# Kernel optimization log

Hardware: AMD Instinct MI355X
Metric: run time of the kernel (lower is better)

## Reference

```python
import jax, jax.numpy as jnp
import numpy as np

BINS = 6  # torch.histc(bins=6, min=0, max=256) in rarity()


def _border_mask(h, w, dtype):
    m = jnp.ones((h, w), dtype)
    return m.at[0, :].set(0).at[-1, :].set(0).at[:, 0].set(0).at[:, -1].set(0)


def _norm(x, lo, hi, axes):
    # normalize_tensor: map to [lo,hi]; all-zeros if constant map
    mn = x.min(axes, keepdims=True)
    mx = x.max(axes, keepdims=True)
    d = mx - mn
    ds = jnp.where(d == 0, jnp.ones_like(d), d)
    out = (x - mn) / ds * (hi - lo) + lo
    return jnp.where(d == 0, jnp.zeros_like(out), out)


def _ponder(x, axes):
    # map_ponderation: normalize to [0,1] then scale by (max-mean)^2
    w = (x.max(axes, keepdims=True) - x.mean(axes, keepdims=True)) ** 2
    return _norm(x, 0.0, 1.0, axes) * w


def _rarity_all(ch):
    # Vectorized rarity() over all channels. ch: [C,H,W]
    C, H, W = ch.shape
    ch = ch * _border_mask(H, W, ch.dtype)          # zero 1-px border
    ch = _norm(ch, 0.0, 256.0, (1, 2))              # per-channel -> [0,256]
    # torch.histc over [0,256]: bin = floor(v*bins/256), max value in last bin
    bin_idx = jnp.clip((ch * (BINS / 256.0)).astype(jnp.int32), 0, BINS - 1)
    hist = jax.nn.one_hot(bin_idx, BINS, dtype=ch.dtype).sum((1, 2))  # [C,BINS]
    hist = hist / hist.sum(-1, keepdims=True)
    hist = -jnp.log(hist + 1e-4)
    # lookup: (channel*bins - 1).long().clamp(0, bins-1)  (channel in [0,256], as in source)
    lut_idx = jnp.clip((ch * BINS - 1).astype(jnp.int32), 0, BINS - 1)
    dst = hist[jnp.arange(C)[:, None, None], lut_idx]  # [C,H,W] rarity lookup
    dst = _norm(dst, 0.0, 1.0, (1, 2))
    return _ponder(dst, (1, 2))


def _apply_rarity(x):
    # x: [1,C,H,W] -> [H,W]
    ch = x[0]
    H, W = ch.shape[-2:]
    r = _rarity_all(ch)
    # channel 0: ponderated again, no extra border zeroing (as in source)
    p0 = _ponder(r[0], (0, 1))
    rest = r[1:] * _border_mask(H, W, r.dtype)  # channels 1..C-1: border zeroed
    p = p0 + _ponder(rest, (1, 2)).sum(0)
    return _norm(p, 0.0, 1.0, (0, 1))  # threshold=None -> no thresholding


def _resize240(m):
    # T.Resize((240,240), bilinear) ~ half-pixel linear resize
    return jax.image.resize(m, (240, 240), method='linear')


def _forward(layers):
    # group layers into packs by spatial resolution (static, shapes known)
    packs = {}
    for t in layers:
        packs.setdefault(t.shape[-2:], []).append(t)
    group_maps = []
    for pack in packs.values():
        maps = [_resize240(_apply_rarity(t)) for t in pack]
        fused = maps[0] * 0.0
        for m in maps:  # fuse_itti
            fused = fused + _ponder(m, (0, 1))
        group_maps.append(_norm(fused, 0.0, 256.0, (0, 1)))
    groups = jnp.stack(group_maps, -1)  # [240,240,n_packs]
    return groups.sum(-1), groups


def setup_inputs() -> dict:
    key = jax.random.key(0)
    shapes = ([(1, 64, 224, 224)] * 2 + [(1, 128, 112, 112)] * 2 +
              [(1, 256, 56, 56)] * 3 + [(1, 512, 28, 28)] * 3 +
              [(1, 512, 14, 14)] * 3)
    keys = jax.random.split(key, len(shapes))
    return {f"x{i}": jax.random.uniform(keys[i], s, jnp.float32)
            for i, s in enumerate(shapes)}


def reference(x0, x1, x2, x3, x4, x5, x6, x7, x8, x9, x10, x11, x12):
    return _forward([x0, x1, x2, x3, x4, x5, x6, x7, x8, x9, x10, x11, x12])
```

## Files before the change

kernel.cpp:

```cpp
#include <hip/hip_runtime.h>
#include <math.h>

#define NT 13
#define RHW 57600
#define PIXB 8192

struct Meta {
  const float* x[NT];
  int C[NT];
  int H[NT];
  float hsc[NT];
  int pixOff[NT + 1];
  int mmOff[NT + 1];
  int nchMM[NT];
  int pmOff[NT + 1];
};

__device__ __forceinline__ int segOf(const int* off, int b) {
  int t = 0;
  while (t + 1 < NT && b >= off[t + 1]) t++;
  return t;
}

template <int HH>
__device__ __forceinline__ void mm_body(const float* __restrict__ ch, int pix0, int pix1, float& mn, float& mx) {
  constexpr int W = HH, H = HH;
  int i40 = pix0 >> 2, i41 = pix1 >> 2;
  for (int i4 = i40 + (int)threadIdx.x; i4 < i41; i4 += 256) {
    float4 v = reinterpret_cast<const float4*>(ch)[i4];
#pragma unroll
    for (int j = 0; j < 4; j++) {
      int idx = i4 * 4 + j;
      int h = idx / W, w = idx - h * W;
      bool ok = h > 0 && h < (H - 1) && w > 0 && w < (W - 1);
      float f = (j == 0) ? v.x : (j == 1) ? v.y : (j == 2) ? v.z : v.w;
      if (ok) { mn = fminf(mn, f); mx = fmaxf(mx, f); }
    }
  }
}

__global__ __launch_bounds__(256) void k_minmax(Meta m, float* cpart) {
  int b = blockIdx.x;
  int t = segOf(m.mmOff, b);
  int local = b - m.mmOff[t];
  int nch = m.nchMM[t];
  int c = local / nch, k = local - c * nch;
  int HW = m.H[t] * m.H[t];
  const float* ch = m.x[t] + (size_t)c * HW;
  int pix0 = k * PIXB, pix1 = min(pix0 + PIXB, HW);
  float mn = INFINITY, mx = -INFINITY;
  switch (m.H[t]) {
    case 224: mm_body<224>(ch, pix0, pix1, mn, mx); break;
    case 112: mm_body<112>(ch, pix0, pix1, mn, mx); break;
    case 56:  mm_body<56>(ch, pix0, pix1, mn, mx); break;
    case 28:  mm_body<28>(ch, pix0, pix1, mn, mx); break;
    default:  mm_body<14>(ch, pix0, pix1, mn, mx); break;
  }
#pragma unroll
  for (int o = 32; o > 0; o >>= 1) {
    mn = fminf(mn, __shfl_down(mn, o));
    mx = fmaxf(mx, __shfl_down(mx, o));
  }
  __shared__ float smn[4], smx[4];
  int wid = threadIdx.x >> 6;
  if ((threadIdx.x & 63) == 0) { smn[wid] = mn; smx[wid] = mx; }
  __syncthreads();
  if (threadIdx.x == 0) {
    for (int i = 1; i < 4; i++) { mn = fminf(mn, smn[i]); mx = fmaxf(mx, smx[i]); }
    cpart[2 * b] = mn; cpart[2 * b + 1] = mx;
  }
}

template <int HH>
__device__ __forceinline__ void hist_body(const float* __restrict__ ch, int pix0, int pix1,
                                          float mn, float invd,
                                          unsigned long long& cbin, unsigned long long& clut) {
  constexpr int W = HH, H = HH;
  int i40 = pix0 >> 2, i41 = pix1 >> 2;
  int nIter = (i41 - i40 + 255) >> 8;
  for (int it = 0; it < nIter; ++it) {
    int i4 = i40 + it * 256 + (int)threadIdx.x;
    bool valid = i4 < i41;
    float4 v = make_float4(0.f, 0.f, 0.f, 0.f);
    if (valid) v = reinterpret_cast<const float4*>(ch)[i4];
#pragma unroll
    for (int j = 0; j < 4; j++) {
      int idx = i4 * 4 + j;
      int h = idx / W, w = idx - h * W;
      bool ok = valid && h > 0 && h < (H - 1) && w > 0 && w < (W - 1);
      float f = (j == 0) ? v.x : (j == 1) ? v.y : (j == 2) ? v.z : v.w;
      float vv = (f - mn) * invd * 256.0f;
      int bin = (int)(vv * 0.0234375f);
      bin = bin < 0 ? 0 : (bin > 5 ? 5 : bin);
      float tt = vv * 6.0f - 1.0f;
      int li = (int)tt;
      li = li < 0 ? 0 : (li > 5 ? 5 : li);
      cbin += (unsigned long long)ok << (bin * 10);
      clut += (unsigned long long)ok << (li * 10);
    }
  }
}

__global__ __launch_bounds__(256) void k_hist(Meta m, const float* cpart, unsigned* hpart) {
  int b = blockIdx.x;
  int t = segOf(m.mmOff, b);
  int local = b - m.mmOff[t];
  int nch = m.nchMM[t];
  int c = local / nch, k = local - c * nch;
  int HW = m.H[t] * m.H[t];
  const float* ch = m.x[t] + (size_t)c * HW;
  int cb = m.mmOff[t] + c * nch;
  float mn = INFINITY, mx = -INFINITY;
  for (int kk = 0; kk < nch; kk++) {
    mn = fminf(mn, cpart[2 * (cb + kk)]);
    mx = fmaxf(mx, cpart[2 * (cb + kk) + 1]);
  }
  mn = fminf(mn, 0.f);
  mx = fmaxf(mx, 0.f);
  float d = mx - mn;
  float invd = d > 0.f ? 1.0f / d : 0.f;
  int pix0 = k * PIXB, pix1 = min(pix0 + PIXB, HW);
  unsigned long long cbin = 0ull, clut = 0ull;
  switch (m.H[t]) {
    case 224: hist_body<224>(ch, pix0, pix1, mn, invd, cbin, clut); break;
    case 112: hist_body<112>(ch, pix0, pix1, mn, invd, cbin, clut); break;
    case 56:  hist_body<56>(ch, pix0, pix1, mn, invd, cbin, clut); break;
    case 28:  hist_body<28>(ch, pix0, pix1, mn, invd, cbin, clut); break;
    default:  hist_body<14>(ch, pix0, pix1, mn, invd, cbin, clut); break;
  }
  unsigned pk[6];
#pragma unroll
  for (int j = 0; j < 6; j++)
    pk[j] = (unsigned)((cbin >> (10 * j)) & 1023ull) | ((unsigned)((clut >> (10 * j)) & 1023ull) << 16);
#pragma unroll
  for (int o = 32; o > 0; o >>= 1) {
#pragma unroll
    for (int j = 0; j < 6; j++) pk[j] += __shfl_down(pk[j], o);
  }
  __shared__ unsigned swh[4][12];
  int wid = threadIdx.x >> 6, lane = threadIdx.x & 63;
  if (lane == 0) {
#pragma unroll
    for (int j = 0; j < 6; j++) { swh[wid][j] = pk[j] & 0xffffu; swh[wid][6 + j] = pk[j] >> 16; }
  }
  __syncthreads();
  if (threadIdx.x < 12)
    hpart[12 * b + threadIdx.x] =
        swh[0][threadIdx.x] + swh[1][threadIdx.x] + swh[2][threadIdx.x] + swh[3][threadIdx.x];
}

template <int HH>
__device__ __forceinline__ void pm_inner(const float* __restrict__ X, int i4, bool act,
                                         int c0, int c1, const float* sLut,
                                         const float* sMn, const float* sInv, float* a) {
  constexpr int W = HH, H = HH;
  constexpr int i4n = (H * W) / 4;
  if (!act) return;
  int bf[4];
#pragma unroll
  for (int j = 0; j < 4; j++) {
    int idx = i4 * 4 + j;
    int h = idx / W, w = idx - h * W;
    bf[j] = (h == 0 || h == H - 1 || w == 0 || w == W - 1) ? 1 : 0;
  }
  const float4* Xp = reinterpret_cast<const float4*>(X);
#pragma unroll 4
  for (int c = c0; c < c1; ++c) {
    float4 v = Xp[(size_t)c * i4n + i4];
    float mnc = sMn[c], ivc = sInv[c];
    const float* L = sLut + c * 8;
    float fv0 = v.x, fv1 = v.y, fv2 = v.z, fv3 = v.w;
    { float vv = (fv0 - mnc) * ivc * 256.0f; float tt = vv * 6.0f - 1.0f; int li = (int)tt; li = li < 0 ? 0 : (li > 5 ? 5 : li); a[0] += L[bf[0] ? 6 : li]; }
    { float vv = (fv1 - mnc) * ivc * 256.0f; float tt = vv * 6.0f - 1.0f; int li = (int)tt; li = li < 0 ? 0 : (li > 5 ? 5 : li); a[1] += L[bf[1] ? 6 : li]; }
    { float vv = (fv2 - mnc) * ivc * 256.0f; float tt = vv * 6.0f - 1.0f; int li = (int)tt; li = li < 0 ? 0 : (li > 5 ? 5 : li); a[2] += L[bf[2] ? 6 : li]; }
    { float vv = (fv3 - mnc) * ivc * 256.0f; float tt = vv * 6.0f - 1.0f; int li = (int)tt; li = li < 0 ? 0 : (li > 5 ? 5 : li); a[3] += L[bf[3] ? 6 : li]; }
  }
}

__global__ __launch_bounds__(512) void k_pmap(Meta m, const float* cpart, const unsigned* hpart,
                                              float* pmaps, float* ppart) {
  __shared__ float sLut[512 * 8];
  __shared__ float sMn[512], sInv[512];
  __shared__ float sAcc[8][256];
  int b = blockIdx.x;
  int t = segOf(m.pmOff, b);
  int blk = b - m.pmOff[t];
  int C = m.C[t], H = m.H[t], W = H, HW = H * W;
  int nch = m.nchMM[t];
  int tid = threadIdx.x;
  if (tid < C) {
    int cb = m.mmOff[t] + tid * nch;
    float mn = INFINITY, mx = -INFINITY;
    unsigned hh[12];
#pragma unroll
    for (int j = 0; j < 12; j++) hh[j] = 0u;
    for (int k = 0; k < nch; k++) {
      mn = fminf(mn, cpart[2 * (cb + k)]);
      mx = fmaxf(mx, cpart[2 * (cb + k) + 1]);
#pragma unroll
      for (int j = 0; j < 12; j++) hh[j] += hpart[12 * (cb + k) + j];
    }
    mn = fminf(mn, 0.f); mx = fmaxf(mx, 0.f);
    float d = mx - mn;
    float invd = d > 0.f ? 1.0f / d : 0.f;
    float fHW = (float)HW;
    int nb = 2 * (H + W) - 4;
    float vb = (0.f - mn) * invd * 256.0f;
    int bin_b = (int)(vb * 0.0234375f);
    bin_b = bin_b < 0 ? 0 : (bin_b > 5 ? 5 : bin_b);
    float ttb = vb * 6.0f - 1.0f;
    int lib = (int)ttb;
    lib = lib < 0 ? 0 : (lib > 5 ? 5 : lib);
    hh[bin_b] += (unsigned)nb;
    hh[6 + lib] += (unsigned)nb;
    float hl[6];
#pragma unroll
    for (int j = 0; j < 6; j++) hl[j] = -logf((float)hh[j] / fHW + 1e-4f);
    float mn2 = INFINITY, mx2 = -INFINITY, sum2 = 0.f;
#pragma unroll
    for (int j = 0; j < 6; j++) {
      unsigned cc = hh[6 + j];
      if (cc) { mn2 = fminf(mn2, hl[j]); mx2 = fmaxf(mx2, hl[j]); sum2 += (float)cc * hl[j]; }
    }
    float d2 = mx2 - mn2;
    float RL[6];
    if (d2 > 0.f) {
      float meanN = (sum2 / fHW - mn2) / d2;
      float w = 1.0f - meanN; w *= w;
#pragma unroll
      for (int j = 0; j < 6; j++) RL[j] = (hl[j] - mn2) / d2 * w;
    } else {
#pragma unroll
      for (int j = 0; j < 6; j++) RL[j] = 0.f;
    }
    float LUT[7];
    if (tid == 0) {
      float mnr = INFINITY, mxr = -INFINITY, sumr = 0.f;
#pragma unroll
      for (int j = 0; j < 6; j++) {
        unsigned cc = hh[6 + j];
        if (cc) { mnr = fminf(mnr, RL[j]); mxr = fmaxf(mxr, RL[j]); sumr += (float)cc * RL[j]; }
      }
      float dr = mxr - mnr;
      if (dr > 0.f) {
        float meanr = sumr / fHW;
        float wp = mxr - meanr; wp *= wp;
#pragma unroll
        for (int j = 0; j < 6; j++) LUT[j] = (RL[j] - mnr) / dr * wp;
        LUT[6] = LUT[lib];
      } else {
#pragma unroll
        for (int j = 0; j < 7; j++) LUT[j] = 0.f;
      }
    } else {
      float mnr = 0.f, mxr = 0.f, sumr = 0.f;
#pragma unroll
      for (int j = 0; j < 6; j++) {
        int cc = (int)hh[6 + j] - (j == lib ? nb : 0);
        if (cc > 0) { mnr = fminf(mnr, RL[j]); mxr = fmaxf(mxr, RL[j]); sumr += (float)cc * RL[j]; }
      }
      float dr = mxr - mnr;
      if (dr > 0.f) {
        float meanr = sumr / fHW;
        float wp = mxr - meanr; wp *= wp;
#pragma unroll
        for (int j = 0; j < 6; j++) LUT[j] = (RL[j] - mnr) / dr * wp;
        LUT[6] = (0.f - mnr) / dr * wp;
      } else {
#pragma unroll
        for (int j = 0; j < 7; j++) LUT[j] = 0.f;
      }
    }
#pragma unroll
    for (int j = 0; j < 7; j++) sLut[tid * 8 + j] = LUT[j];
    sLut[tid * 8 + 7] = 0.f;
    sMn[tid] = mn; sInv[tid] = invd;
  }
  __syncthreads();
  int wid = tid >> 6, lane = tid & 63;
  int i4n = HW >> 2;
  int i4 = blk * 64 + lane;
  bool act = i4 < i4n;
  float a[4] = {0.f, 0.f, 0.f, 0.f};
  int cpw = C >> 3;
  switch (H) {
    case 224: pm_inner<224>(m.x[t], i4, act, wid * cpw, (wid + 1) * cpw, sLut, sMn, sInv, a); break;
    case 112: pm_inner<112>(m.x[t], i4, act, wid * cpw, (wid + 1) * cpw, sLut, sMn, sInv, a); break;
    case 56:  pm_inner<56>(m.x[t], i4, act, wid * cpw, (wid + 1) * cpw, sLut, sMn, sInv, a); break;
    case 28:  pm_inner<28>(m.x[t], i4, act, wid * cpw, (wid + 1) * cpw, sLut, sMn, sInv, a); break;
    default:  pm_inner<14>(m.x[t], i4, act, wid * cpw, (wid + 1) * cpw, sLut, sMn, sInv, a); break;
  }
  *reinterpret_cast<float4*>(&sAcc[wid][lane * 4]) = make_float4(a[0], a[1], a[2], a[3]);
  __syncthreads();
  if (wid == 0) {
    float bmn = INFINITY, bmx = -INFINITY;
    if (act) {
      float t0 = 0.f, t1 = 0.f, t2 = 0.f, t3 = 0.f;
#pragma unroll
      for (int w = 0; w < 8; w++) {
        const float* s = &sAcc[w][lane * 4];
        t0 += s[0]; t1 += s[1]; t2 += s[2]; t3 += s[3];
      }
      size_t o = (size_t)m.pixOff[t] + (size_t)i4 * 4;
      *reinterpret_cast<float4*>(pmaps + o) = make_float4(t0, t1, t2, t3);
      bmn = fminf(fminf(t0, t1), fminf(t2, t3));
      bmx = fmaxf(fmaxf(t0, t1), fmaxf(t2, t3));
    }
#pragma unroll
    for (int o = 32; o > 0; o >>= 1) {
      bmn = fminf(bmn, __shfl_down(bmn, o));
      bmx = fmaxf(bmx, __shfl_down(bmx, o));
    }
    if (lane == 0) { ppart[2 * b] = bmn; ppart[2 * b + 1] = bmx; }
  }
}

__global__ __launch_bounds__(256) void k_resize(Meta m, const float* pmaps, const float* ppart,
                                                float* mmaps, float* rpart) {
  __shared__ float sMnT, sInvT;
  int t = blockIdx.x / 225;
  int blk = blockIdx.x % 225;
  int wid = threadIdx.x >> 6, lane = threadIdx.x & 63;
  if (wid == 0) {
    int n = m.pmOff[t + 1] - m.pmOff[t];
    const float* pp = ppart + (size_t)m.pmOff[t] * 2;
    float mn = INFINITY, mx = -INFINITY;
    for (int i = lane; i < n; i += 64) { mn = fminf(mn, pp[2 * i]); mx = fmaxf(mx, pp[2 * i + 1]); }
#pragma unroll
    for (int o = 32; o > 0; o >>= 1) {
      mn = fminf(mn, __shfl_down(mn, o));
      mx = fmaxf(mx, __shfl_down(mx, o));
    }
    if (lane == 0) {
      float d = mx - mn;
      sMnT = mn; sInvT = d > 0.f ? 1.0f / d : 0.f;
    }
  }
  __syncthreads();
  int pix = blk * 256 + threadIdx.x;
  int H = m.H[t], W = m.H[t];
  const float* p = pmaps + m.pixOff[t];
  float mn = sMnT, a = sInvT;
  int oy = pix / 240, ox = pix - oy * 240;
  float hs = m.hsc[t];
  float sy = ((float)oy + 0.5f) * hs - 0.5f;
  float sx = ((float)ox + 0.5f) * hs - 0.5f;
  float fy0 = floorf(sy), fx0 = floorf(sx);
  float fy = sy - fy0, fx = sx - fx0;
  int iy0 = (int)fy0, ix0 = (int)fx0;
  int y0 = iy0 < 0 ? 0 : (iy0 > H - 1 ? H - 1 : iy0);
  int y1 = iy0 + 1 < 0 ? 0 : (iy0 + 1 > H - 1 ? H - 1 : iy0 + 1);
  int x0 = ix0 < 0 ? 0 : (ix0 > W - 1 ? W - 1 : ix0);
  int x1 = ix0 + 1 < 0 ? 0 : (ix0 + 1 > W - 1 ? W - 1 : ix0 + 1);
  float v00 = p[y0 * W + x0], v01 = p[y0 * W + x1];
  float v10 = p[y1 * W + x0], v11 = p[y1 * W + x1];
  float r = (1.f - fy) * ((1.f - fx) * v00 + fx * v01) + fy * ((1.f - fx) * v10 + fx * v11);
  float mv = (r - mn) * a;
  mmaps[(size_t)t * RHW + pix] = mv;
  float bmn = mv, bmx = mv, bsm = mv;
#pragma unroll
  for (int o = 32; o > 0; o >>= 1) {
    bmn = fminf(bmn, __shfl_down(bmn, o));
    bmx = fmaxf(bmx, __shfl_down(bmx, o));
    bsm += __shfl_down(bsm, o);
  }
  __shared__ float smn[4], smx[4], ssm[4];
  if ((threadIdx.x & 63) == 0) { smn[wid] = bmn; smx[wid] = bmx; ssm[wid] = bsm; }
  __syncthreads();
  if (threadIdx.x == 0) {
    for (int i = 1; i < 4; i++) { bmn = fminf(bmn, smn[i]); bmx = fmaxf(bmx, smx[i]); bsm += ssm[i]; }
    float* rp = rpart + ((size_t)t * 225 + blk) * 3;
    rp[0] = bmn; rp[1] = bmx; rp[2] = bsm;
  }
}

__global__ __launch_bounds__(256) void k_fuse(const float* mmaps, const float* rpart,
                                              float* fusedm, float* fpart) {
  __shared__ float sMn[3], sD[3], sW[3];
  int g = blockIdx.x / 225;
  int blk = blockIdx.x % 225;
  const int gs[6] = {0, 2, 4, 7, 10, 13};
  int nt = gs[g + 1] - gs[g];
  int wid = threadIdx.x >> 6, lane = threadIdx.x & 63;
  if (wid < nt) {
    int t = gs[g] + wid;
    const float* rp = rpart + (size_t)t * 225 * 3;
    float mn = INFINITY, mx = -INFINITY, sm = 0.f;
    for (int i = lane; i < 225; i += 64) {
      mn = fminf(mn, rp[3 * i]); mx = fmaxf(mx, rp[3 * i + 1]); sm += rp[3 * i + 2];
    }
#pragma unroll
    for (int o = 32; o > 0; o >>= 1) {
      mn = fminf(mn, __shfl_down(mn, o));
      mx = fmaxf(mx, __shfl_down(mx, o));
      sm += __shfl_down(sm, o);
    }
    if (lane == 0) {
      float d = mx - mn;
      if (d > 0.f) {
        float mean = sm * (1.0f / 57600.0f);
        float w = mx - mean; w *= w;
        sMn[wid] = mn; sD[wid] = d; sW[wid] = w;
      } else {
        sMn[wid] = 0.f; sD[wid] = 0.f; sW[wid] = 0.f;
      }
    }
  }
  __syncthreads();
  int pix = blk * 256 + threadIdx.x;
  float acc = 0.f;
  for (int k = 0; k < nt; k++) {
    int t = gs[g] + k;
    if (sD[k] > 0.f) acc += (mmaps[(size_t)t * RHW + pix] - sMn[k]) / sD[k] * sW[k];
  }
  fusedm[(size_t)g * RHW + pix] = acc;
  float bmn = acc, bmx = acc;
#pragma unroll
  for (int o = 32; o > 0; o >>= 1) {
    bmn = fminf(bmn, __shfl_down(bmn, o));
    bmx = fmaxf(bmx, __shfl_down(bmx, o));
  }
  __shared__ float smn[4], smx[4];
  if ((threadIdx.x & 63) == 0) { smn[wid] = bmn; smx[wid] = bmx; }
  __syncthreads();
  if (threadIdx.x == 0) {
    for (int i = 1; i < 4; i++) { bmn = fminf(bmn, smn[i]); bmx = fmaxf(bmx, smx[i]); }
    float* fp = fpart + ((size_t)g * 225 + blk) * 2;
    fp[0] = bmn; fp[1] = bmx;
  }
}

__global__ __launch_bounds__(256) void k_out(const float* fusedm, const float* fpart, float* out) {
  __shared__ float fmn[5], finv[5];
  int wid = threadIdx.x >> 6, lane = threadIdx.x & 63;
  for (int g = wid; g < 5; g += 4) {
    const float* fp = fpart + (size_t)g * 225 * 2;
    float mn = INFINITY, mx = -INFINITY;
    for (int i = lane; i < 225; i += 64) {
      mn = fminf(mn, fp[2 * i]); mx = fmaxf(mx, fp[2 * i + 1]);
    }
#pragma unroll
    for (int o = 32; o > 0; o >>= 1) {
      mn = fminf(mn, __shfl_down(mn, o));
      mx = fmaxf(mx, __shfl_down(mx, o));
    }
    if (lane == 0) {
      float d = mx - mn;
      fmn[g] = mn; finv[g] = d > 0.f ? 256.0f / d : 0.f;
    }
  }
  __syncthreads();
  int pix = blockIdx.x * 256 + threadIdx.x;
  float acc = 0.f;
  float* out2 = out + RHW;
#pragma unroll
  for (int g = 0; g < 5; g++) {
    float v = (fusedm[(size_t)g * RHW + pix] - fmn[g]) * finv[g];
    out2[(size_t)pix * 5 + g] = v;
    acc += v;
  }
  out[pix] = acc;
}

extern "C" void kernel_launch(void* const* d_in, const int* in_sizes, int n_in,
                              void* d_out, int out_size, void* d_ws, size_t ws_size,
                              hipStream_t stream) {
  static const int Cs[NT] = {64, 64, 128, 128, 256, 256, 256, 512, 512, 512, 512, 512, 512};
  static const int Hs[NT] = {224, 224, 112, 112, 56, 56, 56, 28, 28, 28, 14, 14, 14};
  Meta m;
  int po = 0, mmb = 0, pmb = 0;
  for (int t = 0; t < NT; t++) {
    m.x[t] = (const float*)d_in[t];
    m.C[t] = Cs[t]; m.H[t] = Hs[t];
    m.hsc[t] = (float)((double)Hs[t] / 240.0);
    int HW = Hs[t] * Hs[t];
    m.pixOff[t] = po; po += HW;
    m.mmOff[t] = mmb;
    m.nchMM[t] = (HW + PIXB - 1) / PIXB;
    mmb += Cs[t] * m.nchMM[t];
    m.pmOff[t] = pmb;
    pmb += (HW + 255) / 256;
  }
  m.pixOff[NT] = po; m.mmOff[NT] = mmb; m.pmOff[NT] = pmb;

  size_t off = 0;
  auto a16 = [](size_t x) { return (x + 15) & ~(size_t)15; };
#define WALLOC(var, type, count) type* var = (type*)((char*)d_ws + off); off = a16(off + sizeof(type) * (size_t)(count));
  WALLOC(cpart, float, 2 * mmb)
  WALLOC(hpart, unsigned, 12 * mmb)
  WALLOC(ppart, float, 2 * pmb)
  WALLOC(rpart, float, NT * 225 * 3)
  WALLOC(fpart, float, 5 * 225 * 2)
  WALLOC(pmaps, float, po)
  WALLOC(mmaps, float, NT * RHW)
  WALLOC(fusedm, float, 5 * RHW)
#undef WALLOC

  hipLaunchKernelGGL(k_minmax, dim3(mmb), dim3(256), 0, stream, m, cpart);
  hipLaunchKernelGGL(k_hist, dim3(mmb), dim3(256), 0, stream, m, cpart, hpart);
  hipLaunchKernelGGL(k_pmap, dim3(pmb), dim3(512), 0, stream, m, cpart, hpart, pmaps, ppart);
  hipLaunchKernelGGL(k_resize, dim3(NT * 225), dim3(256), 0, stream, m, pmaps, ppart, mmaps, rpart);
  hipLaunchKernelGGL(k_fuse, dim3(5 * 225), dim3(256), 0, stream, mmaps, rpart, fusedm, fpart);
  hipLaunchKernelGGL(k_out, dim3(225), dim3(256), 0, stream, fusedm, fpart, (float*)d_out);
}
```

Baseline: 77.44 us.

## Fuse per-channel minmax, histogram and LUT into one kernel; emit packed 3-bit bin indices

Merges the minmax and histogram kernels into a single per-channel kernel of 512 threads. That kernel reads each channel twice, computes the rarity LUT once per channel, and writes a packed 4-bit-per-pixel LUT index map. The pmap kernel then reads these 16-bit nibble packs instead of the full float inputs, which cuts its global traffic by about 8x. It also no longer recomputes the LUT from partials in every block. In exchange, there are fewer blocks in the channel kernel (one per channel), a serial LUT computation on thread 0, and a new intermediate buffer write.

```diff
diff --git a/kernel.cpp b/kernel.cpp
--- a/kernel.cpp
+++ b/kernel.cpp
@@ -3,16 +3,17 @@
 
 #define NT 13
 #define RHW 57600
-#define PIXB 8192
+
+typedef unsigned long long ull;
 
 struct Meta {
   const float* x[NT];
   int C[NT];
   int H[NT];
   float hsc[NT];
+  int chanOff[NT + 1];
   int pixOff[NT + 1];
-  int mmOff[NT + 1];
-  int nchMM[NT];
+  int nibOff[NT];
   int pmOff[NT + 1];
 };
 
@@ -23,10 +24,10 @@
 }
 
 template <int HH>
-__device__ __forceinline__ void mm_body(const float* __restrict__ ch, int pix0, int pix1, float& mn, float& mx) {
+__device__ __forceinline__ void mmA(const float* __restrict__ ch, float& mn, float& mx) {
   constexpr int W = HH, H = HH;
-  int i40 = pix0 >> 2, i41 = pix1 >> 2;
-  for (int i4 = i40 + (int)threadIdx.x; i4 < i41; i4 += 256) {
+  constexpr int f4n = (H * W) / 4;
+  for (int i4 = (int)threadIdx.x; i4 < f4n; i4 += 512) {
     float4 v = reinterpret_cast<const float4*>(ch)[i4];
 #pragma unroll
     for (int j = 0; j < 4; j++) {
@@ -39,55 +40,19 @@
   }
 }
 
-__global__ __launch_bounds__(256) void k_minmax(Meta m, float* cpart) {
-  int b = blockIdx.x;
-  int t = segOf(m.mmOff, b);
-  int local = b - m.mmOff[t];
-  int nch = m.nchMM[t];
-  int c = local / nch, k = local - c * nch;
-  int HW = m.H[t] * m.H[t];
-  const float* ch = m.x[t] + (size_t)c * HW;
-  int pix0 = k * PIXB, pix1 = min(pix0 + PIXB, HW);
-  float mn = INFINITY, mx = -INFINITY;
-  switch (m.H[t]) {
-    case 224: mm_body<224>(ch, pix0, pix1, mn, mx); break;
-    case 112: mm_body<112>(ch, pix0, pix1, mn, mx); break;
-    case 56:  mm_body<56>(ch, pix0, pix1, mn, mx); break;
-    case 28:  mm_body<28>(ch, pix0, pix1, mn, mx); break;
-    default:  mm_body<14>(ch, pix0, pix1, mn, mx); break;
-  }
-#pragma unroll
-  for (int o = 32; o > 0; o >>= 1) {
-    mn = fminf(mn, __shfl_down(mn, o));
-    mx = fmaxf(mx, __shfl_down(mx, o));
-  }
-  __shared__ float smn[4], smx[4];
-  int wid = threadIdx.x >> 6;
-  if ((threadIdx.x & 63) == 0) { smn[wid] = mn; smx[wid] = mx; }
-  __syncthreads();
-  if (threadIdx.x == 0) {
-    for (int i = 1; i < 4; i++) { mn = fminf(mn, smn[i]); mx = fmaxf(mx, smx[i]); }
-    cpart[2 * b] = mn; cpart[2 * b + 1] = mx;
-  }
-}
-
 template <int HH>
-__device__ __forceinline__ void hist_body(const float* __restrict__ ch, int pix0, int pix1,
-                                          float mn, float invd,
-                                          unsigned long long& cbin, unsigned long long& clut) {
+__device__ __forceinline__ void histB(const float* __restrict__ ch, unsigned short* __restrict__ nb,
+                                      float mn, float invd, ull& cbin, ull& clut) {
   constexpr int W = HH, H = HH;
-  int i40 = pix0 >> 2, i41 = pix1 >> 2;
-  int nIter = (i41 - i40 + 255) >> 8;
-  for (int it = 0; it < nIter; ++it) {
-    int i4 = i40 + it * 256 + (int)threadIdx.x;
-    bool valid = i4 < i41;
-    float4 v = make_float4(0.f, 0.f, 0.f, 0.f);
-    if (valid) v = reinterpret_cast<const float4*>(ch)[i4];
+  constexpr int f4n = (H * W) / 4;
+  for (int i4 = (int)threadIdx.x; i4 < f4n; i4 += 512) {
+    float4 v = reinterpret_cast<const float4*>(ch)[i4];
+    unsigned pack = 0;
 #pragma unroll
     for (int j = 0; j < 4; j++) {
       int idx = i4 * 4 + j;
       int h = idx / W, w = idx - h * W;
-      bool ok = valid && h > 0 && h < (H - 1) && w > 0 && w < (W - 1);
+      bool intr = h > 0 && h < (H - 1) && w > 0 && w < (W - 1);
       float f = (j == 0) ? v.x : (j == 1) ? v.y : (j == 2) ? v.z : v.w;
       float vv = (f - mn) * invd * 256.0f;
       int bin = (int)(vv * 0.0234375f);
@@ -95,214 +60,205 @@
       float tt = vv * 6.0f - 1.0f;
       int li = (int)tt;
       li = li < 0 ? 0 : (li > 5 ? 5 : li);
-      cbin += (unsigned long long)ok << (bin * 10);
-      clut += (unsigned long long)ok << (li * 10);
-    }
-  }
-}
-
-__global__ __launch_bounds__(256) void k_hist(Meta m, const float* cpart, unsigned* hpart) {
+      cbin += (ull)intr << (bin * 10);
+      clut += (ull)intr << (li * 10);
+      pack |= (unsigned)(intr ? li : 7) << (4 * j);
+    }
+    nb[i4] = (unsigned short)pack;
+  }
+}
+
+__device__ __forceinline__ void lutMath(int c, int H, int HW, float mn, float invd,
+                                        unsigned* hh, float* LUT ) {
+  float fHW = (float)HW;
+  int nbp = 4 * H - 4;
+  float vb = (0.f - mn) * invd * 256.0f;
+  int bin_b = (int)(vb * 0.0234375f);
+  bin_b = bin_b < 0 ? 0 : (bin_b > 5 ? 5 : bin_b);
+  float ttb = vb * 6.0f - 1.0f;
+  int lib = (int)ttb;
+  lib = lib < 0 ? 0 : (lib > 5 ? 5 : lib);
+  hh[bin_b] += (unsigned)nbp;
+  hh[6 + lib] += (unsigned)nbp;
+  float hl[6];
+#pragma unroll
+  for (int j = 0; j < 6; j++) hl[j] = -logf((float)hh[j] / fHW + 1e-4f);
+  float mn2 = INFINITY, mx2 = -INFINITY, sum2 = 0.f;
+#pragma unroll
+  for (int j = 0; j < 6; j++) {
+    unsigned cc = hh[6 + j];
+    if (cc) { mn2 = fminf(mn2, hl[j]); mx2 = fmaxf(mx2, hl[j]); sum2 += (float)cc * hl[j]; }
+  }
+  float d2 = mx2 - mn2;
+  float RL[6];
+  if (d2 > 0.f) {
+    float meanN = (sum2 / fHW - mn2) / d2;
+    float w = 1.0f - meanN; w *= w;
+#pragma unroll
+    for (int j = 0; j < 6; j++) RL[j] = (hl[j] - mn2) / d2 * w;
+  } else {
+#pragma unroll
+    for (int j = 0; j < 6; j++) RL[j] = 0.f;
+  }
+  if (c == 0) {
+    float mnr = INFINITY, mxr = -INFINITY, sumr = 0.f;
+#pragma unroll
+    for (int j = 0; j < 6; j++) {
+      unsigned cc = hh[6 + j];
+      if (cc) { mnr = fminf(mnr, RL[j]); mxr = fmaxf(mxr, RL[j]); sumr += (float)cc * RL[j]; }
+    }
+    float dr = mxr - mnr;
+    if (dr > 0.f) {
+      float meanr = sumr / fHW;
+      float wp = mxr - meanr; wp *= wp;
+#pragma unroll
+      for (int j = 0; j < 6; j++) LUT[j] = (RL[j] - mnr) / dr * wp;
+      LUT[6] = LUT[lib];
+    } else {
+#pragma unroll
+      for (int j = 0; j < 7; j++) LUT[j] = 0.f;
+    }
+  } else {
+    float mnr = 0.f, mxr = 0.f, sumr = 0.f;
+#pragma unroll
+    for (int j = 0; j < 6; j++) {
+      int cc = (int)hh[6 + j] - (j == lib ? nbp : 0);
+      if (cc > 0) { mnr = fminf(mnr, RL[j]); mxr = fmaxf(mxr, RL[j]); sumr += (float)cc * RL[j]; }
+    }
+    float dr = mxr - mnr;
+    if (dr > 0.f) {
+      float meanr = sumr / fHW;
+      float wp = mxr - meanr; wp *= wp;
+#pragma unroll
+      for (int j = 0; j < 6; j++) LUT[j] = (RL[j] - mnr) / dr * wp;
+      LUT[6] = (0.f - mnr) / dr * wp;
+    } else {
+#pragma unroll
+      for (int j = 0; j < 7; j++) LUT[j] = 0.f;
+    }
+  }
+}
+
+__global__ __launch_bounds__(512) void k_chan(Meta m, unsigned short* __restrict__ nib,
+                                              float* __restrict__ lutg) {
   int b = blockIdx.x;
-  int t = segOf(m.mmOff, b);
-  int local = b - m.mmOff[t];
-  int nch = m.nchMM[t];
-  int c = local / nch, k = local - c * nch;
-  int HW = m.H[t] * m.H[t];
+  int t = segOf(m.chanOff, b);
+  int c = b - m.chanOff[t];
+  int H = m.H[t], HW = H * H;
   const float* ch = m.x[t] + (size_t)c * HW;
-  int cb = m.mmOff[t] + c * nch;
+  int tid = threadIdx.x, wid = tid >> 6, lane = tid & 63;
+
   float mn = INFINITY, mx = -INFINITY;
-  for (int kk = 0; kk < nch; kk++) {
-    mn = fminf(mn, cpart[2 * (cb + kk)]);
-    mx = fmaxf(mx, cpart[2 * (cb + kk) + 1]);
-  }
-  mn = fminf(mn, 0.f);
-  mx = fmaxf(mx, 0.f);
-  float d = mx - mn;
-  float invd = d > 0.f ? 1.0f / d : 0.f;
-  int pix0 = k * PIXB, pix1 = min(pix0 + PIXB, HW);
-  unsigned long long cbin = 0ull, clut = 0ull;
-  switch (m.H[t]) {
-    case 224: hist_body<224>(ch, pix0, pix1, mn, invd, cbin, clut); break;
-    case 112: hist_body<112>(ch, pix0, pix1, mn, invd, cbin, clut); break;
-    case 56:  hist_body<56>(ch, pix0, pix1, mn, invd, cbin, clut); break;
-    case 28:  hist_body<28>(ch, pix0, pix1, mn, invd, cbin, clut); break;
-    default:  hist_body<14>(ch, pix0, pix1, mn, invd, cbin, clut); break;
+  switch (H) {
+    case 224: mmA<224>(ch, mn, mx); break;
+    case 112: mmA<112>(ch, mn, mx); break;
+    case 56:  mmA<56>(ch, mn, mx); break;
+    case 28:  mmA<28>(ch, mn, mx); break;
+    default:  mmA<14>(ch, mn, mx); break;
+  }
+#pragma unroll
+  for (int o = 32; o > 0; o >>= 1) {
+    mn = fminf(mn, __shfl_down(mn, o));
+    mx = fmaxf(mx, __shfl_down(mx, o));
+  }
+  __shared__ float smn[8], smx[8];
+  __shared__ float sMn, sInv;
+  if (lane == 0) { smn[wid] = mn; smx[wid] = mx; }
+  __syncthreads();
+  if (tid == 0) {
+    for (int i = 1; i < 8; i++) { mn = fminf(mn, smn[i]); mx = fmaxf(mx, smx[i]); }
+    mn = fminf(mn, 0.f); mx = fmaxf(mx, 0.f);
+    float d = mx - mn;
+    sMn = mn; sInv = d > 0.f ? 1.0f / d : 0.f;
+  }
+  __syncthreads();
+  float mnc = sMn, invd = sInv;
+
+  unsigned short* nb = nib + m.nibOff[t] + (size_t)c * (HW >> 2);
+  ull cbin = 0ull, clut = 0ull;
+  switch (H) {
+    case 224: histB<224>(ch, nb, mnc, invd, cbin, clut); break;
+    case 112: histB<112>(ch, nb, mnc, invd, cbin, clut); break;
+    case 56:  histB<56>(ch, nb, mnc, invd, cbin, clut); break;
+    case 28:  histB<28>(ch, nb, mnc, invd, cbin, clut); break;
+    default:  histB<14>(ch, nb, mnc, invd, cbin, clut); break;
   }
   unsigned pk[6];
 #pragma unroll
   for (int j = 0; j < 6; j++)
-    pk[j] = (unsigned)((cbin >> (10 * j)) & 1023ull) | ((unsigned)((clut >> (10 * j)) & 1023ull) << 16);
+    pk[j] = (unsigned)((cbin >> (10 * j)) & 1023ull) |
+            ((unsigned)((clut >> (10 * j)) & 1023ull) << 16);
 #pragma unroll
   for (int o = 32; o > 0; o >>= 1) {
 #pragma unroll
     for (int j = 0; j < 6; j++) pk[j] += __shfl_down(pk[j], o);
   }
-  __shared__ unsigned swh[4][12];
-  int wid = threadIdx.x >> 6, lane = threadIdx.x & 63;
+  __shared__ unsigned spk[8][6];
   if (lane == 0) {
 #pragma unroll
-    for (int j = 0; j < 6; j++) { swh[wid][j] = pk[j] & 0xffffu; swh[wid][6 + j] = pk[j] >> 16; }
-  }
-  __syncthreads();
-  if (threadIdx.x < 12)
-    hpart[12 * b + threadIdx.x] =
-        swh[0][threadIdx.x] + swh[1][threadIdx.x] + swh[2][threadIdx.x] + swh[3][threadIdx.x];
-}
-
-template <int HH>
-__device__ __forceinline__ void pm_inner(const float* __restrict__ X, int i4, bool act,
-                                         int c0, int c1, const float* sLut,
-                                         const float* sMn, const float* sInv, float* a) {
-  constexpr int W = HH, H = HH;
-  constexpr int i4n = (H * W) / 4;
-  if (!act) return;
-  int bf[4];
-#pragma unroll
-  for (int j = 0; j < 4; j++) {
-    int idx = i4 * 4 + j;
-    int h = idx / W, w = idx - h * W;
-    bf[j] = (h == 0 || h == H - 1 || w == 0 || w == W - 1) ? 1 : 0;
-  }
-  const float4* Xp = reinterpret_cast<const float4*>(X);
-#pragma unroll 4
-  for (int c = c0; c < c1; ++c) {
-    float4 v = Xp[(size_t)c * i4n + i4];
-    float mnc = sMn[c], ivc = sInv[c];
-    const float* L = sLut + c * 8;
-    float fv0 = v.x, fv1 = v.y, fv2 = v.z, fv3 = v.w;
-    { float vv = (fv0 - mnc) * ivc * 256.0f; float tt = vv * 6.0f - 1.0f; int li = (int)tt; li = li < 0 ? 0 : (li > 5 ? 5 : li); a[0] += L[bf[0] ? 6 : li]; }
-    { float vv = (fv1 - mnc) * ivc * 256.0f; float tt = vv * 6.0f - 1.0f; int li = (int)tt; li = li < 0 ? 0 : (li > 5 ? 5 : li); a[1] += L[bf[1] ? 6 : li]; }
-    { float vv = (fv2 - mnc) * ivc * 256.0f; float tt = vv * 6.0f - 1.0f; int li = (int)tt; li = li < 0 ? 0 : (li > 5 ? 5 : li); a[2] += L[bf[2] ? 6 : li]; }
-    { float vv = (fv3 - mnc) * ivc * 256.0f; float tt = vv * 6.0f - 1.0f; int li = (int)tt; li = li < 0 ? 0 : (li > 5 ? 5 : li); a[3] += L[bf[3] ? 6 : li]; }
-  }
-}
-
-__global__ __launch_bounds__(512) void k_pmap(Meta m, const float* cpart, const unsigned* hpart,
-                                              float* pmaps, float* ppart) {
+    for (int j = 0; j < 6; j++) spk[wid][j] = pk[j];
+  }
+  __syncthreads();
+  if (tid == 0) {
+    unsigned hh[12];
+#pragma unroll
+    for (int j = 0; j < 6; j++) {
+      unsigned s = 0;
+#pragma unroll
+      for (int w = 0; w < 8; w++) s += spk[w][j];
+      hh[j] = s & 0xffffu; hh[6 + j] = s >> 16;
+    }
+    float LUT[7];
+    lutMath(c, H, HW, mnc, invd, hh, LUT);
+    float* o = lutg + (size_t)b * 8;
+#pragma unroll
+    for (int j = 0; j < 6; j++) o[j] = LUT[j];
+    o[6] = LUT[6]; o[7] = LUT[6];
+  }
+}
+
+__global__ __launch_bounds__(256) void k_pmap(Meta m, const unsigned short* __restrict__ nib,
+                                              const float* __restrict__ lutg,
+                                              float* __restrict__ pmaps, float* __restrict__ ppart) {
   __shared__ float sLut[512 * 8];
-  __shared__ float sMn[512], sInv[512];
-  __shared__ float sAcc[8][256];
+  __shared__ float sAcc[4][256];
   int b = blockIdx.x;
   int t = segOf(m.pmOff, b);
   int blk = b - m.pmOff[t];
-  int C = m.C[t], H = m.H[t], W = H, HW = H * W;
-  int nch = m.nchMM[t];
-  int tid = threadIdx.x;
-  if (tid < C) {
-    int cb = m.mmOff[t] + tid * nch;
-    float mn = INFINITY, mx = -INFINITY;
-    unsigned hh[12];
-#pragma unroll
-    for (int j = 0; j < 12; j++) hh[j] = 0u;
-    for (int k = 0; k < nch; k++) {
-      mn = fminf(mn, cpart[2 * (cb + k)]);
-      mx = fmaxf(mx, cpart[2 * (cb + k) + 1]);
-#pragma unroll
-      for (int j = 0; j < 12; j++) hh[j] += hpart[12 * (cb + k) + j];
-    }
-    mn = fminf(mn, 0.f); mx = fmaxf(mx, 0.f);
-    float d = mx - mn;
-    float invd = d > 0.f ? 1.0f / d : 0.f;
-    float fHW = (float)HW;
-    int nb = 2 * (H + W) - 4;
-    float vb = (0.f - mn) * invd * 256.0f;
-    int bin_b = (int)(vb * 0.0234375f);
-    bin_b = bin_b < 0 ? 0 : (bin_b > 5 ? 5 : bin_b);
-    float ttb = vb * 6.0f - 1.0f;
-    int lib = (int)ttb;
-    lib = lib < 0 ? 0 : (lib > 5 ? 5 : lib);
-    hh[bin_b] += (unsigned)nb;
-    hh[6 + lib] += (unsigned)nb;
-    float hl[6];
-#pragma unroll
-    for (int j = 0; j < 6; j++) hl[j] = -logf((float)hh[j] / fHW + 1e-4f);
-    float mn2 = INFINITY, mx2 = -INFINITY, sum2 = 0.f;
-#pragma unroll
-    for (int j = 0; j < 6; j++) {
-      unsigned cc = hh[6 + j];
-      if (cc) { mn2 = fminf(mn2, hl[j]); mx2 = fmaxf(mx2, hl[j]); sum2 += (float)cc * hl[j]; }
-    }
-    float d2 = mx2 - mn2;
-    float RL[6];
-    if (d2 > 0.f) {
-      float meanN = (sum2 / fHW - mn2) / d2;
-      float w = 1.0f - meanN; w *= w;
-#pragma unroll
-      for (int j = 0; j < 6; j++) RL[j] = (hl[j] - mn2) / d2 * w;
-    } else {
-#pragma unroll
-      for (int j = 0; j < 6; j++) RL[j] = 0.f;
-    }
-    float LUT[7];
-    if (tid == 0) {
-      float mnr = INFINITY, mxr = -INFINITY, sumr = 0.f;
-#pragma unroll
-      for (int j = 0; j < 6; j++) {
-        unsigned cc = hh[6 + j];
-        if (cc) { mnr = fminf(mnr, RL[j]); mxr = fmaxf(mxr, RL[j]); sumr += (float)cc * RL[j]; }
-      }
-      float dr = mxr - mnr;
-      if (dr > 0.f) {
-        float meanr = sumr / fHW;
-        float wp = mxr - meanr; wp *= wp;
-#pragma unroll
-        for (int j = 0; j < 6; j++) LUT[j] = (RL[j] - mnr) / dr * wp;
-        LUT[6] = LUT[lib];
-      } else {
-#pragma unroll
-        for (int j = 0; j < 7; j++) LUT[j] = 0.f;
-      }
-    } else {
-      float mnr = 0.f, mxr = 0.f, sumr = 0.f;
-#pragma unroll
-      for (int j = 0; j < 6; j++) {
-        int cc = (int)hh[6 + j] - (j == lib ? nb : 0);
-        if (cc > 0) { mnr = fminf(mnr, RL[j]); mxr = fmaxf(mxr, RL[j]); sumr += (float)cc * RL[j]; }
-      }
-      float dr = mxr - mnr;
-      if (dr > 0.f) {
-        float meanr = sumr / fHW;
-        float wp = mxr - meanr; wp *= wp;
-#pragma unroll
-        for (int j = 0; j < 6; j++) LUT[j] = (RL[j] - mnr) / dr * wp;
-        LUT[6] = (0.f - mnr) / dr * wp;
-      } else {
-#pragma unroll
-        for (int j = 0; j < 7; j++) LUT[j] = 0.f;
-      }
-    }
-#pragma unroll
-    for (int j = 0; j < 7; j++) sLut[tid * 8 + j] = LUT[j];
-    sLut[tid * 8 + 7] = 0.f;
-    sMn[tid] = mn; sInv[tid] = invd;
-  }
-  __syncthreads();
-  int wid = tid >> 6, lane = tid & 63;
-  int i4n = HW >> 2;
+  int C = m.C[t], HW = m.H[t] * m.H[t], i4n = HW >> 2;
+  int tid = threadIdx.x, wid = tid >> 6, lane = tid & 63;
+  const float4* Lg = reinterpret_cast<const float4*>(lutg + (size_t)m.chanOff[t] * 8);
+  for (int i = tid; i < C * 2; i += 256) reinterpret_cast<float4*>(sLut)[i] = Lg[i];
+  __syncthreads();
   int i4 = blk * 64 + lane;
   bool act = i4 < i4n;
-  float a[4] = {0.f, 0.f, 0.f, 0.f};
-  int cpw = C >> 3;
-  switch (H) {
-    case 224: pm_inner<224>(m.x[t], i4, act, wid * cpw, (wid + 1) * cpw, sLut, sMn, sInv, a); break;
-    case 112: pm_inner<112>(m.x[t], i4, act, wid * cpw, (wid + 1) * cpw, sLut, sMn, sInv, a); break;
-    case 56:  pm_inner<56>(m.x[t], i4, act, wid * cpw, (wid + 1) * cpw, sLut, sMn, sInv, a); break;
-    case 28:  pm_inner<28>(m.x[t], i4, act, wid * cpw, (wid + 1) * cpw, sLut, sMn, sInv, a); break;
-    default:  pm_inner<14>(m.x[t], i4, act, wid * cpw, (wid + 1) * cpw, sLut, sMn, sInv, a); break;
-  }
-  *reinterpret_cast<float4*>(&sAcc[wid][lane * 4]) = make_float4(a[0], a[1], a[2], a[3]);
+  float a0 = 0.f, a1 = 0.f, a2 = 0.f, a3 = 0.f;
+  if (act) {
+    const unsigned short* nb = nib + m.nibOff[t] + i4;
+    int cpw = C >> 2;
+    int c0 = wid * cpw, c1 = c0 + cpw;
+#pragma unroll 4
+    for (int c = c0; c < c1; ++c) {
+      unsigned n = nb[(size_t)c * i4n];
+      a0 += sLut[c * 8 + (int)(n & 7u)];
+      a1 += sLut[c * 8 + (int)((n >> 4) & 7u)];
+      a2 += sLut[c * 8 + (int)((n >> 8) & 7u)];
+      a3 += sLut[c * 8 + (int)((n >> 12) & 7u)];
+    }
+  }
+  *reinterpret_cast<float4*>(&sAcc[wid][lane * 4]) = make_float4(a0, a1, a2, a3);
   __syncthreads();
   if (wid == 0) {
     float bmn = INFINITY, bmx = -INFINITY;
     if (act) {
       float t0 = 0.f, t1 = 0.f, t2 = 0.f, t3 = 0.f;
 #pragma unroll
-      for (int w = 0; w < 8; w++) {
+      for (int w = 0; w < 4; w++) {
         const float* s = &sAcc[w][lane * 4];
         t0 += s[0]; t1 += s[1]; t2 += s[2]; t3 += s[3];
       }
-      size_t o = (size_t)m.pixOff[t] + (size_t)i4 * 4;
-      *reinterpret_cast<float4*>(pmaps + o) = make_float4(t0, t1, t2, t3);
+      *reinterpret_cast<float4*>(pmaps + (size_t)m.pixOff[t] + (size_t)i4 * 4) =
+          make_float4(t0, t1, t2, t3);
       bmn = fminf(fminf(t0, t1), fminf(t2, t3));
       bmx = fmaxf(fmaxf(t0, t1), fmaxf(t2, t3));
     }
@@ -468,26 +424,24 @@
   static const int Cs[NT] = {64, 64, 128, 128, 256, 256, 256, 512, 512, 512, 512, 512, 512};
   static const int Hs[NT] = {224, 224, 112, 112, 56, 56, 56, 28, 28, 28, 14, 14, 14};
   Meta m;
-  int po = 0, mmb = 0, pmb = 0;
+  int co = 0, po = 0, pmb = 0, nibTot = 0;
   for (int t = 0; t < NT; t++) {
     m.x[t] = (const float*)d_in[t];
     m.C[t] = Cs[t]; m.H[t] = Hs[t];
     m.hsc[t] = (float)((double)Hs[t] / 240.0);
     int HW = Hs[t] * Hs[t];
+    m.chanOff[t] = co; co += Cs[t];
     m.pixOff[t] = po; po += HW;
-    m.mmOff[t] = mmb;
-    m.nchMM[t] = (HW + PIXB - 1) / PIXB;
-    mmb += Cs[t] * m.nchMM[t];
-    m.pmOff[t] = pmb;
-    pmb += (HW + 255) / 256;
-  }
-  m.pixOff[NT] = po; m.mmOff[NT] = mmb; m.pmOff[NT] = pmb;
+    m.nibOff[t] = nibTot; nibTot += Cs[t] * (HW >> 2);
+    m.pmOff[t] = pmb; pmb += (HW + 255) / 256;
+  }
+  m.chanOff[NT] = co; m.pixOff[NT] = po; m.pmOff[NT] = pmb;
 
   size_t off = 0;
   auto a16 = [](size_t x) { return (x + 15) & ~(size_t)15; };
 #define WALLOC(var, type, count) type* var = (type*)((char*)d_ws + off); off = a16(off + sizeof(type) * (size_t)(count));
-  WALLOC(cpart, float, 2 * mmb)
-  WALLOC(hpart, unsigned, 12 * mmb)
+  WALLOC(nib, unsigned short, nibTot)
+  WALLOC(lutg, float, 8 * co)
   WALLOC(ppart, float, 2 * pmb)
   WALLOC(rpart, float, NT * 225 * 3)
   WALLOC(fpart, float, 5 * 225 * 2)
@@ -496,9 +450,8 @@
   WALLOC(fusedm, float, 5 * RHW)
 #undef WALLOC
 
-  hipLaunchKernelGGL(k_minmax, dim3(mmb), dim3(256), 0, stream, m, cpart);
-  hipLaunchKernelGGL(k_hist, dim3(mmb), dim3(256), 0, stream, m, cpart, hpart);
-  hipLaunchKernelGGL(k_pmap, dim3(pmb), dim3(512), 0, stream, m, cpart, hpart, pmaps, ppart);
+  hipLaunchKernelGGL(k_chan, dim3(co), dim3(512), 0, stream, m, nib, lutg);
+  hipLaunchKernelGGL(k_pmap, dim3(pmb), dim3(256), 0, stream, m, nib, lutg, pmaps, ppart);
   hipLaunchKernelGGL(k_resize, dim3(NT * 225), dim3(256), 0, stream, m, pmaps, ppart, mmaps, rpart);
   hipLaunchKernelGGL(k_fuse, dim3(5 * 225), dim3(256), 0, stream, mmaps, rpart, fusedm, fpart);
   hipLaunchKernelGGL(k_out, dim3(225), dim3(256), 0, stream, fusedm, fpart, (float*)d_out);
```

Result: faster. 75.55 us (-2.4%).
